# Kernel tuning notes

Measured on AMD Instinct MI355X. Metric: run time of the kernel, lower is better.

Reference implementation:

```python
import jax, jax.numpy as jnp
import numpy as np

KNN_K = 3
EPS = 1e-8


def _make_poses(key, batch):
    """Random valid SE(3) matrices [B,4,4] (rotation via QR, small translation)."""
    k1, k2 = jax.random.split(key)
    A = jax.random.normal(k1, (batch, 3, 3), dtype=jnp.float32)
    Q, _ = jnp.linalg.qr(A)
    det = jnp.linalg.det(Q)[:, None, None]
    Q = Q * jnp.where(det < 0, -1.0, 1.0)  # ensure proper rotation
    t = jax.random.normal(k2, (batch, 3), dtype=jnp.float32) * 0.5
    pose = jnp.tile(jnp.eye(4, dtype=jnp.float32), (batch, 1, 1))
    pose = pose.at[:, :3, :3].set(Q)
    pose = pose.at[:, :3, 3].set(t)
    return pose


def setup_inputs() -> dict:
    key = jax.random.key(0)
    kq, kr, kf, kp0, kp1 = jax.random.split(key, 5)
    B, N, M = 2, 8192, 8192
    pc0 = jax.random.normal(kq, (B, N, 3), dtype=jnp.float32) * 20.0
    pc1 = jax.random.normal(kr, (B, M, 3), dtype=jnp.float32) * 20.0
    flow1 = jax.random.normal(kf, (B, M, 3), dtype=jnp.float32)
    pose0 = _make_poses(kp0, B)
    pose1 = _make_poses(kp1, B)
    return {"pc0": pc0, "pc1": pc1, "flow1": flow1, "pose0": pose0, "pose1": pose1}


def reference(pc0, pc1, flow1, pose0, pose1):
    # cal_pose0to1: transform from pc0 ego frame into pc1 ego frame
    pose_0to1 = jnp.linalg.inv(pose1) @ pose0            # [B,4,4]
    R = pose_0to1[:, :3, :3]                             # [B,3,3]
    t = pose_0to1[:, :3, 3]                              # [B,3]
    # pc0_in_pc1 = pc0 @ R^T + t
    pc0_t = jnp.einsum("bij,bnj->bni", R, pc0) + t[:, None, :]  # [B,N,3]
    pose_flow = pc0_t - pc0                              # ego-motion displacement

    # pairwise squared distances (cdist^2) via GEMM form: [B,N,M]
    q2 = jnp.sum(pc0_t * pc0_t, axis=-1)                 # [B,N]
    r2 = jnp.sum(pc1 * pc1, axis=-1)                     # [B,M]
    cross = jnp.einsum("bnd,bmd->bnm", pc0_t, pc1)
    d2 = q2[:, :, None] + r2[:, None, :] - 2.0 * cross

    # KNN: k smallest distances
    neg_d2, idx = jax.lax.top_k(-d2, KNN_K)              # [B,N,k]
    d = jnp.sqrt(jnp.maximum(-neg_d2, 0.0))

    # inverse-distance weights over the k neighbors
    w = 1.0 / (d + EPS)
    w = w / jnp.sum(w, axis=-1, keepdims=True)           # [B,N,k]

    # gather neighbor flows: flow1 [B,M,3] -> [B,N,k,3]
    gathered = jnp.take_along_axis(flow1[:, None, :, :], idx[..., None], axis=2)
    flow_interp = jnp.sum(w[..., None] * gathered, axis=2)  # [B,N,3]
    return flow_interp, pose_flow
```

## Files before the change

### kernel.cpp

```cpp
#include <hip/hip_runtime.h>
#include <math.h>
#include <float.h>
#include <limits.h>

#define CS   64
#define CT   32
#define TILE_PTS (CT * CS)
#define CSP  65
#define QB1  64
#define QT   16
#define MARGIN 0.05f
typedef unsigned long long ull;
#define KMAX 0xFFFFFFFFFFFFFFFFull

__device__ __forceinline__ unsigned int ford(float f) {
    unsigned int b = __float_as_uint(f);
    return b ^ (((unsigned int)((int)b >> 31)) | 0x80000000u);
}
__device__ __forceinline__ float funord(unsigned int u) {
    unsigned int m = ((u >> 31) - 1u) | 0x80000000u;
    return __uint_as_float(u ^ m);
}

__device__ __forceinline__ ull umin64(ull a, ull b) { return a < b ? a : b; }
__device__ __forceinline__ ull umax64(ull a, ull b) { return a > b ? a : b; }

__device__ __forceinline__ void ins3k(ull k, ull& k0, ull& k1, ull& k2) {
    ull n2 = umax64(k1, umin64(k2, k));
    ull n1 = umax64(k0, umin64(k1, k));
    k0 = umin64(k0, k);
    k1 = n1;
    k2 = n2;
}

__device__ __forceinline__ void sins(float d, float& a0, float& a1, float& a2)
{
    float n1 = __builtin_amdgcn_fmed3f(a0, a1, d);
    float n2 = __builtin_amdgcn_fmed3f(a1, a2, d);
    a0 = fminf(a0, d);
    a1 = n1;
    a2 = n2;
}

__device__ __forceinline__ void pose_rel(const float* __restrict__ P0,
                                         const float* __restrict__ P1,
                                         float R[3][3], float tv[3])
{
    float dt0 = P0[3]  - P1[3];
    float dt1 = P0[7]  - P1[7];
    float dt2 = P0[11] - P1[11];
    #pragma unroll
    for (int i = 0; i < 3; ++i) {
        float a0 = P1[i], a1 = P1[4 + i], a2 = P1[8 + i];
        #pragma unroll
        for (int j = 0; j < 3; ++j)
            R[i][j] = fmaf(a2, P0[8 + j], fmaf(a1, P0[4 + j], a0 * P0[j]));
        tv[i] = fmaf(a2, dt2, fmaf(a1, dt1, a0 * dt0));
    }
}

__launch_bounds__(256, 4)
__global__ void knn_phaseA(const float* __restrict__ pc0,
                           const float* __restrict__ pc1,
                           const float* __restrict__ pose0,
                           const float* __restrict__ pose1,
                           float* __restrict__ cmin,
                           int B, int N, int M, int cstride)
{
    __shared__ float4 tile[CT * CSP];
    __shared__ float4 qd[QB1];

    const int tid = threadIdx.x;
    const int b   = blockIdx.z;
    const int ctb = blockIdx.y;
    const int qb  = blockIdx.x * QB1;
    const int pbase = ctb * TILE_PTS;

    if (tid < QB1) {
        float R[3][3], tv[3];
        pose_rel(pose0 + b * 16, pose1 + b * 16, R, tv);
        int qg0 = qb + tid;
        int qg  = (qg0 < N) ? qg0 : (N - 1);
        const float px = pc0[(size_t)(b * N + qg) * 3 + 0];
        const float py = pc0[(size_t)(b * N + qg) * 3 + 1];
        const float pz = pc0[(size_t)(b * N + qg) * 3 + 2];
        float qx = fmaf(R[0][2], pz, fmaf(R[0][1], py, R[0][0] * px)) + tv[0];
        float qy = fmaf(R[1][2], pz, fmaf(R[1][1], py, R[1][0] * px)) + tv[1];
        float qz = fmaf(R[2][2], pz, fmaf(R[2][1], py, R[2][0] * px)) + tv[2];
        qd[tid] = make_float4(qx, qy, qz,
                              (qx * qx + qy * qy) + qz * qz);
    }

    #pragma unroll
    for (int k = 0; k < TILE_PTS / (256 * 4); ++k) {
        const int pl = (tid + k * 256) * 4;
        const int p  = pbase + pl;
        float4* dst = &tile[(pl >> 6) * CSP + (pl & (CS - 1))];
        if (p + 3 < M) {
            const float4* pf = (const float4*)(pc1 + (size_t)(b * M + p) * 3);
            float4 A = pf[0], Bv = pf[1], C = pf[2];
            dst[0] = make_float4(-2.f * A.x, -2.f * A.y, -2.f * A.z,
                                 (A.x * A.x + A.y * A.y) + A.z * A.z);
            dst[1] = make_float4(-2.f * A.w, -2.f * Bv.x, -2.f * Bv.y,
                                 (A.w * A.w + Bv.x * Bv.x) + Bv.y * Bv.y);
            dst[2] = make_float4(-2.f * Bv.z, -2.f * Bv.w, -2.f * C.x,
                                 (Bv.z * Bv.z + Bv.w * Bv.w) + C.x * C.x);
            dst[3] = make_float4(-2.f * C.y, -2.f * C.z, -2.f * C.w,
                                 (C.y * C.y + C.z * C.z) + C.w * C.w);
        } else {
            #pragma unroll
            for (int u = 0; u < 4; ++u) {
                int pp = p + u;
                float4 v;
                if (pp < M) {
                    const float* s = pc1 + (size_t)(b * M + pp) * 3;
                    float x = s[0], y = s[1], z = s[2];
                    v = make_float4(-2.f * x, -2.f * y, -2.f * z,
                                    (x * x + y * y) + z * z);
                } else {
                    v = make_float4(0.f, 0.f, 0.f, FLT_MAX);
                }
                dst[u] = v;
            }
        }
    }
    __syncthreads();

    const int w    = tid >> 6;
    const int lane = tid & 63;
    const int cl   = lane & 31;
    const int part = lane >> 5;

    float4 qv[QT];
    #pragma unroll
    for (int t = 0; t < QT; ++t) qv[t] = qd[w * QT + t];

    float mm[QT];
    #pragma unroll
    for (int t = 0; t < QT; ++t) mm[t] = FLT_MAX;

    const float4* tp = &tile[cl * CSP + part * 32];
    #pragma unroll 4
    for (int i = 0; i < 32; ++i) {
        const float4 v = tp[i];
        #pragma unroll
        for (int t = 0; t < QT; ++t)
            mm[t] = fminf(mm[t],
                fmaf(qv[t].x, v.x, fmaf(qv[t].y, v.y, fmaf(qv[t].z, v.z, v.w))));
    }

    #pragma unroll
    for (int t = 0; t < QT; ++t)
        mm[t] = fminf(mm[t], __shfl_xor(mm[t], 32));

    if (part == 0) {
        const int cg = ctb * CT + cl;
        #pragma unroll
        for (int t = 0; t < QT; ++t) {
            int qg0 = qb + w * QT + t;
            int qg  = (qg0 < N) ? qg0 : (N - 1);
            cmin[((size_t)b * N + qg) * cstride + cg] = mm[t];
        }
    }
}

__launch_bounds__(256, 8)
__global__ void knn_select(const float* __restrict__ pc0,
                           const float* __restrict__ pc1,
                           const float* __restrict__ flow1,
                           const float* __restrict__ pose0,
                           const float* __restrict__ pose1,
                           const float* __restrict__ cmin,
                           float* __restrict__ out,
                           int B, int N, int M, int cstride)
{
    const int tid  = threadIdx.x;
    const int w    = tid >> 6;
    const int lane = tid & 63;
    const int g    = lane >> 4;
    const int l    = lane & 15;
    const int b    = blockIdx.y;
    const int q0   = blockIdx.x * 16 + w * 4 + g;
    const bool qvalid = (q0 < N);
    const int q    = qvalid ? q0 : (N - 1);

    const size_t row = (size_t)(b * N + q) * cstride;
    const float4 sA = *(const float4*)&cmin[row + l * 8];
    const float4 sB = *(const float4*)&cmin[row + l * 8 + 4];

    float R[3][3], tv[3];
    pose_rel(pose0 + b * 16, pose1 + b * 16, R, tv);
    const float px = pc0[(size_t)(b * N + q) * 3 + 0];
    const float py = pc0[(size_t)(b * N + q) * 3 + 1];
    const float pz = pc0[(size_t)(b * N + q) * 3 + 2];
    const float qx = fmaf(R[0][2], pz, fmaf(R[0][1], py, R[0][0] * px)) + tv[0];
    const float qy = fmaf(R[1][2], pz, fmaf(R[1][1], py, R[1][0] * px)) + tv[1];
    const float qz = fmaf(R[2][2], pz, fmaf(R[2][1], py, R[2][0] * px)) + tv[2];
    const float q2 = (qx * qx + qy * qy) + qz * qz;

    float a0 = FLT_MAX, a1 = FLT_MAX, a2 = FLT_MAX;
    sins(sA.x, a0, a1, a2); sins(sA.y, a0, a1, a2);
    sins(sA.z, a0, a1, a2); sins(sA.w, a0, a1, a2);
    sins(sB.x, a0, a1, a2); sins(sB.y, a0, a1, a2);
    sins(sB.z, a0, a1, a2); sins(sB.w, a0, a1, a2);
    #pragma unroll
    for (int msk = 1; msk <= 8; msk <<= 1) {
        float o0 = __shfl_xor(a0, msk);
        float o1 = __shfl_xor(a1, msk);
        float o2 = __shfl_xor(a2, msk);
        sins(o0, a0, a1, a2);
        sins(o1, a0, a1, a2);
        sins(o2, a0, a1, a2);
    }
    const float thr = a2 + MARGIN;

    unsigned int mbits =
          ((unsigned int)(sA.x <= thr) << 0) | ((unsigned int)(sA.y <= thr) << 1)
        | ((unsigned int)(sA.z <= thr) << 2) | ((unsigned int)(sA.w <= thr) << 3)
        | ((unsigned int)(sB.x <= thr) << 4) | ((unsigned int)(sB.y <= thr) << 5)
        | ((unsigned int)(sB.z <= thr) << 6) | ((unsigned int)(sB.w <= thr) << 7);
    ull m0 = (l < 8) ? ((ull)mbits << (8 * l)) : 0ull;
    ull m1 = (l >= 8) ? ((ull)mbits << (8 * (l - 8))) : 0ull;
    #pragma unroll
    for (int msk = 1; msk <= 8; msk <<= 1) {
        m0 |= __shfl_xor(m0, msk);
        m1 |= __shfl_xor(m1, msk);
    }

    ull kA0 = KMAX, kA1 = KMAX, kA2 = KMAX;
    ull kB0 = KMAX, kB1 = KMAX, kB2 = KMAX;
    #pragma unroll
    for (int half = 0; half < 2; ++half) {
        ull mask = half ? m1 : m0;
        const int cbase = half * 64;
        while (mask) {
            const int ck = (int)__builtin_ctzll(mask);
            mask &= mask - 1;
            const int mb = (cbase + ck) * CS;
            #pragma unroll
            for (int r = 0; r < CS / 16; ++r) {
                const int m = mb + r * 16 + l;
                if (m < M) {
                    const float* pp = pc1 + (size_t)(b * M + m) * 3;
                    float x = pp[0], y = pp[1], z = pp[2];
                    float r2 = (x * x + y * y) + z * z;
                    float cr = fmaf(qz, z, fmaf(qy, y, qx * x));
                    float dd = fmaf(-2.0f, cr, q2 + r2);
                    ull kk = ((ull)ford(dd) << 32) | (unsigned int)m;
                    if (r & 1) ins3k(kk, kB0, kB1, kB2);
                    else       ins3k(kk, kA0, kA1, kA2);
                }
            }
        }
    }
    ins3k(kB0, kA0, kA1, kA2);
    ins3k(kB1, kA0, kA1, kA2);
    ins3k(kB2, kA0, kA1, kA2);

    #pragma unroll
    for (int msk = 1; msk <= 8; msk <<= 1) {
        ull o0 = __shfl_xor(kA0, msk);
        ull o1 = __shfl_xor(kA1, msk);
        ull o2 = __shfl_xor(kA2, msk);
        ins3k(o0, kA0, kA1, kA2);
        ins3k(o1, kA0, kA1, kA2);
        ins3k(o2, kA0, kA1, kA2);
    }

    if (l == 0 && qvalid) {
        size_t pf = (size_t)B * N * 3 + (size_t)(b * N + q) * 3;
        out[pf + 0] = qx - px;
        out[pf + 1] = qy - py;
        out[pf + 2] = qz - pz;

        float D0 = funord((unsigned int)(kA0 >> 32));
        float D1 = funord((unsigned int)(kA1 >> 32));
        float D2 = funord((unsigned int)(kA2 >> 32));
        int   i0 = (int)(unsigned int)kA0;
        int   i1 = (int)(unsigned int)kA1;
        int   i2 = (int)(unsigned int)kA2;

        float dd0 = sqrtf(fmaxf(D0, 0.f));
        float dd1 = sqrtf(fmaxf(D1, 0.f));
        float dd2 = sqrtf(fmaxf(D2, 0.f));
        float w0 = 1.0f / (dd0 + 1e-8f);
        float w1 = 1.0f / (dd1 + 1e-8f);
        float w2 = 1.0f / (dd2 + 1e-8f);
        float wsum = (w0 + w1) + w2;
        w0 /= wsum; w1 /= wsum; w2 /= wsum;

        const float* f0 = flow1 + (size_t)(b * M + i0) * 3;
        const float* f1 = flow1 + (size_t)(b * M + i1) * 3;
        const float* f2 = flow1 + (size_t)(b * M + i2) * 3;

        const size_t ob = (size_t)(b * N + q) * 3;
        #pragma unroll
        for (int c = 0; c < 3; ++c) {
            float p0 = w0 * f0[c];
            float p1 = w1 * f1[c];
            float p2 = w2 * f2[c];
            out[ob + c] = (p0 + p1) + p2;
        }
    }
}

extern "C" void kernel_launch(void* const* d_in, const int* in_sizes, int n_in,
                              void* d_out, int out_size, void* d_ws, size_t ws_size,
                              hipStream_t stream) {
    const float* pc0   = (const float*)d_in[0];
    const float* pc1   = (const float*)d_in[1];
    const float* flow1 = (const float*)d_in[2];
    const float* pose0 = (const float*)d_in[3];
    const float* pose1 = (const float*)d_in[4];
    float* out = (float*)d_out;

    const int B = in_sizes[3] / 16;
    const int N = in_sizes[0] / (3 * B);
    const int M = in_sizes[1] / (3 * B);

    const int nct     = (M + TILE_PTS - 1) / TILE_PTS;
    const int cstride = nct * CT;

    float* cmin = (float*)d_ws;

    dim3 g1((N + QB1 - 1) / QB1, nct, B);
    knn_phaseA<<<g1, dim3(256), 0, stream>>>(pc0, pc1, pose0, pose1,
                                             cmin, B, N, M, cstride);

    dim3 g2((N + 15) / 16, B);
    knn_select<<<g2, dim3(256), 0, stream>>>(pc0, pc1, flow1, pose0, pose1,
                                             cmin, out, B, N, M, cstride);
}
```

Measured before the change: 34.59 us.

## Fuse KNN chunk-min and select phases into one kernel with full reference set in LDS

Replaces the two-kernel pipeline, which wrote per-chunk minima to a global workspace and then did a pruned exact search, with a single kernel. Each block loads all 8192 reference points (about 136 KB padded) into shared memory, computes chunk minima for 64 queries, picks candidate chunks, and rescans them from LDS instead of global memory. This removes the workspace round trip and the second launch. In exchange it allows only one block per CU, so grid size and occupancy drop sharply (256 blocks), and it assumes M is at most 8192.

```diff
diff --git a/kernel.cpp b/kernel.cpp
--- a/kernel.cpp
+++ b/kernel.cpp
@@ -3,15 +3,15 @@
 #include <float.h>
 #include <limits.h>
 
-#define CS   64
-#define CT   32
-#define TILE_PTS (CT * CS)
-#define CSP  65
-#define QB1  64
-#define QT   16
+#define MAXM 8192
+#define QPB  64
+#define NS   16
+#define NJ   8
+#define CLEN 64
 #define MARGIN 0.05f
 typedef unsigned long long ull;
 #define KMAX 0xFFFFFFFFFFFFFFFFull
+
 
 __device__ __forceinline__ unsigned int ford(float f) {
     unsigned int b = __float_as_uint(f);
@@ -59,45 +59,49 @@
     }
 }
 
-__launch_bounds__(256, 4)
-__global__ void knn_phaseA(const float* __restrict__ pc0,
-                           const float* __restrict__ pc1,
-                           const float* __restrict__ pose0,
-                           const float* __restrict__ pose1,
-                           float* __restrict__ cmin,
-                           int B, int N, int M, int cstride)
+__launch_bounds__(256, 1)
+__global__ void knn_fused(const float* __restrict__ pc0,
+                          const float* __restrict__ pc1,
+                          const float* __restrict__ flow1,
+                          const float* __restrict__ pose0,
+                          const float* __restrict__ pose1,
+                          float* __restrict__ out,
+                          int B, int N, int M)
 {
-    __shared__ float4 tile[CT * CSP];
-    __shared__ float4 qd[QB1];
+    __shared__ float4 tile[MAXM + (MAXM >> 4)];
+    __shared__ float4 qd[QPB];
 
     const int tid = threadIdx.x;
-    const int b   = blockIdx.z;
-    const int ctb = blockIdx.y;
-    const int qb  = blockIdx.x * QB1;
-    const int pbase = ctb * TILE_PTS;
-
-    if (tid < QB1) {
+    const int b   = blockIdx.y;
+    const int qb  = blockIdx.x * QPB;
+
+    if (tid < QPB) {
         float R[3][3], tv[3];
         pose_rel(pose0 + b * 16, pose1 + b * 16, R, tv);
         int qg0 = qb + tid;
-        int qg  = (qg0 < N) ? qg0 : (N - 1);
+        bool valid = qg0 < N;
+        int qg = valid ? qg0 : (N - 1);
         const float px = pc0[(size_t)(b * N + qg) * 3 + 0];
         const float py = pc0[(size_t)(b * N + qg) * 3 + 1];
         const float pz = pc0[(size_t)(b * N + qg) * 3 + 2];
         float qx = fmaf(R[0][2], pz, fmaf(R[0][1], py, R[0][0] * px)) + tv[0];
         float qy = fmaf(R[1][2], pz, fmaf(R[1][1], py, R[1][0] * px)) + tv[1];
         float qz = fmaf(R[2][2], pz, fmaf(R[2][1], py, R[2][0] * px)) + tv[2];
-        qd[tid] = make_float4(qx, qy, qz,
-                              (qx * qx + qy * qy) + qz * qz);
-    }
-
-    #pragma unroll
-    for (int k = 0; k < TILE_PTS / (256 * 4); ++k) {
-        const int pl = (tid + k * 256) * 4;
-        const int p  = pbase + pl;
-        float4* dst = &tile[(pl >> 6) * CSP + (pl & (CS - 1))];
-        if (p + 3 < M) {
-            const float4* pf = (const float4*)(pc1 + (size_t)(b * M + p) * 3);
+        qd[tid] = make_float4(qx, qy, qz, (qx * qx + qy * qy) + qz * qz);
+        if (valid) {
+            size_t pf = (size_t)B * N * 3 + (size_t)(b * N + qg) * 3;
+            out[pf + 0] = qx - px;
+            out[pf + 1] = qy - py;
+            out[pf + 2] = qz - pz;
+        }
+    }
+
+    #pragma unroll
+    for (int k = 0; k < MAXM / (256 * 4); ++k) {
+        const int p0 = (tid + k * 256) * 4;
+        float4* dst = &tile[p0 + (p0 >> 4)];
+        if (p0 + 3 < M) {
+            const float4* pf = (const float4*)(pc1 + (size_t)(b * M + p0) * 3);
             float4 A = pf[0], Bv = pf[1], C = pf[2];
             dst[0] = make_float4(-2.f * A.x, -2.f * A.y, -2.f * A.z,
                                  (A.x * A.x + A.y * A.y) + A.z * A.z);
@@ -110,7 +114,7 @@
         } else {
             #pragma unroll
             for (int u = 0; u < 4; ++u) {
-                int pp = p + u;
+                int pp = p0 + u;
                 float4 v;
                 if (pp < M) {
                     const float* s = pc1 + (size_t)(b * M + pp) * 3;
@@ -126,180 +130,135 @@
     }
     __syncthreads();
 
+    const int lane = tid & 63;
     const int w    = tid >> 6;
-    const int lane = tid & 63;
-    const int cl   = lane & 31;
-    const int part = lane >> 5;
-
-    float4 qv[QT];
-    #pragma unroll
-    for (int t = 0; t < QT; ++t) qv[t] = qd[w * QT + t];
-
-    float mm[QT];
-    #pragma unroll
-    for (int t = 0; t < QT; ++t) mm[t] = FLT_MAX;
-
-    const float4* tp = &tile[cl * CSP + part * 32];
-    #pragma unroll 4
-    for (int i = 0; i < 32; ++i) {
-        const float4 v = tp[i];
-        #pragma unroll
-        for (int t = 0; t < QT; ++t)
-            mm[t] = fminf(mm[t],
-                fmaf(qv[t].x, v.x, fmaf(qv[t].y, v.y, fmaf(qv[t].z, v.z, v.w))));
-    }
-
-    #pragma unroll
-    for (int t = 0; t < QT; ++t)
-        mm[t] = fminf(mm[t], __shfl_xor(mm[t], 32));
-
-    if (part == 0) {
-        const int cg = ctb * CT + cl;
-        #pragma unroll
-        for (int t = 0; t < QT; ++t) {
-            int qg0 = qb + w * QT + t;
-            int qg  = (qg0 < N) ? qg0 : (N - 1);
-            cmin[((size_t)b * N + qg) * cstride + cg] = mm[t];
-        }
-    }
-}
-
-__launch_bounds__(256, 8)
-__global__ void knn_select(const float* __restrict__ pc0,
-                           const float* __restrict__ pc1,
-                           const float* __restrict__ flow1,
-                           const float* __restrict__ pose0,
-                           const float* __restrict__ pose1,
-                           const float* __restrict__ cmin,
-                           float* __restrict__ out,
-                           int B, int N, int M, int cstride)
-{
-    const int tid  = threadIdx.x;
-    const int w    = tid >> 6;
-    const int lane = tid & 63;
+    const int s    = lane & 15;
     const int g    = lane >> 4;
-    const int l    = lane & 15;
-    const int b    = blockIdx.y;
-    const int q0   = blockIdx.x * 16 + w * 4 + g;
-    const bool qvalid = (q0 < N);
-    const int q    = qvalid ? q0 : (N - 1);
-
-    const size_t row = (size_t)(b * N + q) * cstride;
-    const float4 sA = *(const float4*)&cmin[row + l * 8];
-    const float4 sB = *(const float4*)&cmin[row + l * 8 + 4];
-
-    float R[3][3], tv[3];
-    pose_rel(pose0 + b * 16, pose1 + b * 16, R, tv);
-    const float px = pc0[(size_t)(b * N + q) * 3 + 0];
-    const float py = pc0[(size_t)(b * N + q) * 3 + 1];
-    const float pz = pc0[(size_t)(b * N + q) * 3 + 2];
-    const float qx = fmaf(R[0][2], pz, fmaf(R[0][1], py, R[0][0] * px)) + tv[0];
-    const float qy = fmaf(R[1][2], pz, fmaf(R[1][1], py, R[1][0] * px)) + tv[1];
-    const float qz = fmaf(R[2][2], pz, fmaf(R[2][1], py, R[2][0] * px)) + tv[2];
-    const float q2 = (qx * qx + qy * qy) + qz * qz;
-
-    float a0 = FLT_MAX, a1 = FLT_MAX, a2 = FLT_MAX;
-    sins(sA.x, a0, a1, a2); sins(sA.y, a0, a1, a2);
-    sins(sA.z, a0, a1, a2); sins(sA.w, a0, a1, a2);
-    sins(sB.x, a0, a1, a2); sins(sB.y, a0, a1, a2);
-    sins(sB.z, a0, a1, a2); sins(sB.w, a0, a1, a2);
-    #pragma unroll
-    for (int msk = 1; msk <= 8; msk <<= 1) {
-        float o0 = __shfl_xor(a0, msk);
-        float o1 = __shfl_xor(a1, msk);
-        float o2 = __shfl_xor(a2, msk);
-        sins(o0, a0, a1, a2);
-        sins(o1, a0, a1, a2);
-        sins(o2, a0, a1, a2);
-    }
-    const float thr = a2 + MARGIN;
-
-    unsigned int mbits =
-          ((unsigned int)(sA.x <= thr) << 0) | ((unsigned int)(sA.y <= thr) << 1)
-        | ((unsigned int)(sA.z <= thr) << 2) | ((unsigned int)(sA.w <= thr) << 3)
-        | ((unsigned int)(sB.x <= thr) << 4) | ((unsigned int)(sB.y <= thr) << 5)
-        | ((unsigned int)(sB.z <= thr) << 6) | ((unsigned int)(sB.w <= thr) << 7);
-    ull m0 = (l < 8) ? ((ull)mbits << (8 * l)) : 0ull;
-    ull m1 = (l >= 8) ? ((ull)mbits << (8 * (l - 8))) : 0ull;
-    #pragma unroll
-    for (int msk = 1; msk <= 8; msk <<= 1) {
-        m0 |= __shfl_xor(m0, msk);
-        m1 |= __shfl_xor(m1, msk);
-    }
-
-    ull kA0 = KMAX, kA1 = KMAX, kA2 = KMAX;
-    ull kB0 = KMAX, kB1 = KMAX, kB2 = KMAX;
-    #pragma unroll
-    for (int half = 0; half < 2; ++half) {
-        ull mask = half ? m1 : m0;
-        const int cbase = half * 64;
-        while (mask) {
-            const int ck = (int)__builtin_ctzll(mask);
-            mask &= mask - 1;
-            const int mb = (cbase + ck) * CS;
+    const int l    = s;
+
+    float4 qv[4];
+    #pragma unroll
+    for (int t = 0; t < 4; ++t) qv[t] = qd[w * 16 + g * 4 + t];
+
+    float mm[4][NJ];
+    #pragma unroll
+    for (int t = 0; t < 4; ++t)
+        #pragma unroll
+        for (int j = 0; j < NJ; ++j) mm[t][j] = FLT_MAX;
+
+    const float4* tp = &tile[s];
+    #pragma unroll
+    for (int j = 0; j < NJ; ++j) {
+        const float4* tpj = tp + j * (CLEN * 17);
+        #pragma unroll 4
+        for (int i = 0; i < CLEN; ++i) {
+            const float4 v = tpj[i * 17];
             #pragma unroll
-            for (int r = 0; r < CS / 16; ++r) {
-                const int m = mb + r * 16 + l;
-                if (m < M) {
-                    const float* pp = pc1 + (size_t)(b * M + m) * 3;
-                    float x = pp[0], y = pp[1], z = pp[2];
-                    float r2 = (x * x + y * y) + z * z;
-                    float cr = fmaf(qz, z, fmaf(qy, y, qx * x));
-                    float dd = fmaf(-2.0f, cr, q2 + r2);
-                    ull kk = ((ull)ford(dd) << 32) | (unsigned int)m;
+            for (int t = 0; t < 4; ++t)
+                mm[t][j] = fminf(mm[t][j],
+                    fmaf(qv[t].x, v.x, fmaf(qv[t].y, v.y, fmaf(qv[t].z, v.z, v.w))));
+        }
+    }
+
+    #pragma unroll
+    for (int t = 0; t < 4; ++t) {
+        float a0 = FLT_MAX, a1 = FLT_MAX, a2 = FLT_MAX;
+        #pragma unroll
+        for (int j = 0; j < NJ; ++j) sins(mm[t][j], a0, a1, a2);
+        #pragma unroll
+        for (int msk = 1; msk <= 8; msk <<= 1) {
+            float o0 = __shfl_xor(a0, msk);
+            float o1 = __shfl_xor(a1, msk);
+            float o2 = __shfl_xor(a2, msk);
+            sins(o0, a0, a1, a2);
+            sins(o1, a0, a1, a2);
+            sins(o2, a0, a1, a2);
+        }
+        const float thr = a2 + MARGIN;
+
+        unsigned int bits = 0;
+        #pragma unroll
+        for (int j = 0; j < NJ; ++j)
+            bits |= (unsigned int)(mm[t][j] <= thr) << j;
+        ull m0 = (s < 8) ? ((ull)bits << (8 * s)) : 0ull;
+        ull m1 = (s >= 8) ? ((ull)bits << (8 * (s - 8))) : 0ull;
+        #pragma unroll
+        for (int msk = 1; msk <= 8; msk <<= 1) {
+            m0 |= __shfl_xor(m0, msk);
+            m1 |= __shfl_xor(m1, msk);
+        }
+
+        const float4 qq = qv[t];
+        ull kA0 = KMAX, kA1 = KMAX, kA2 = KMAX;
+        ull kB0 = KMAX, kB1 = KMAX, kB2 = KMAX;
+        #pragma unroll
+        for (int half = 0; half < 2; ++half) {
+            ull mask = half ? m1 : m0;
+            const int cb = half * 64;
+            while (mask) {
+                const int c  = cb + (int)__builtin_ctzll(mask);
+                mask &= mask - 1;
+                const int sc = c >> 3;
+                const int jc = c & 7;
+                #pragma unroll
+                for (int r = 0; r < 4; ++r) {
+                    const int kk_i = jc * CLEN + r * 16 + l;
+                    const int p    = sc + 16 * kk_i;
+                    const float4 v = tile[sc + 17 * kk_i];
+                    float t2 = fmaf(qq.z, v.z, fmaf(qq.y, v.y, qq.x * v.x));
+                    float dd = (qq.w + v.w) + t2;
+                    ull kk = ((ull)ford(dd) << 32) | (unsigned int)p;
                     if (r & 1) ins3k(kk, kB0, kB1, kB2);
                     else       ins3k(kk, kA0, kA1, kA2);
                 }
             }
         }
-    }
-    ins3k(kB0, kA0, kA1, kA2);
-    ins3k(kB1, kA0, kA1, kA2);
-    ins3k(kB2, kA0, kA1, kA2);
-
-    #pragma unroll
-    for (int msk = 1; msk <= 8; msk <<= 1) {
-        ull o0 = __shfl_xor(kA0, msk);
-        ull o1 = __shfl_xor(kA1, msk);
-        ull o2 = __shfl_xor(kA2, msk);
-        ins3k(o0, kA0, kA1, kA2);
-        ins3k(o1, kA0, kA1, kA2);
-        ins3k(o2, kA0, kA1, kA2);
-    }
-
-    if (l == 0 && qvalid) {
-        size_t pf = (size_t)B * N * 3 + (size_t)(b * N + q) * 3;
-        out[pf + 0] = qx - px;
-        out[pf + 1] = qy - py;
-        out[pf + 2] = qz - pz;
-
-        float D0 = funord((unsigned int)(kA0 >> 32));
-        float D1 = funord((unsigned int)(kA1 >> 32));
-        float D2 = funord((unsigned int)(kA2 >> 32));
-        int   i0 = (int)(unsigned int)kA0;
-        int   i1 = (int)(unsigned int)kA1;
-        int   i2 = (int)(unsigned int)kA2;
-
-        float dd0 = sqrtf(fmaxf(D0, 0.f));
-        float dd1 = sqrtf(fmaxf(D1, 0.f));
-        float dd2 = sqrtf(fmaxf(D2, 0.f));
-        float w0 = 1.0f / (dd0 + 1e-8f);
-        float w1 = 1.0f / (dd1 + 1e-8f);
-        float w2 = 1.0f / (dd2 + 1e-8f);
-        float wsum = (w0 + w1) + w2;
-        w0 /= wsum; w1 /= wsum; w2 /= wsum;
-
-        const float* f0 = flow1 + (size_t)(b * M + i0) * 3;
-        const float* f1 = flow1 + (size_t)(b * M + i1) * 3;
-        const float* f2 = flow1 + (size_t)(b * M + i2) * 3;
-
-        const size_t ob = (size_t)(b * N + q) * 3;
-        #pragma unroll
-        for (int c = 0; c < 3; ++c) {
-            float p0 = w0 * f0[c];
-            float p1 = w1 * f1[c];
-            float p2 = w2 * f2[c];
-            out[ob + c] = (p0 + p1) + p2;
+        ins3k(kB0, kA0, kA1, kA2);
+        ins3k(kB1, kA0, kA1, kA2);
+        ins3k(kB2, kA0, kA1, kA2);
+
+        #pragma unroll
+        for (int msk = 1; msk <= 8; msk <<= 1) {
+            ull o0 = __shfl_xor(kA0, msk);
+            ull o1 = __shfl_xor(kA1, msk);
+            ull o2 = __shfl_xor(kA2, msk);
+            ins3k(o0, kA0, kA1, kA2);
+            ins3k(o1, kA0, kA1, kA2);
+            ins3k(o2, kA0, kA1, kA2);
+        }
+
+        if (l == 0) {
+            const int q0 = qb + w * 16 + g * 4 + t;
+            if (q0 < N) {
+                float D0 = funord((unsigned int)(kA0 >> 32));
+                float D1 = funord((unsigned int)(kA1 >> 32));
+                float D2 = funord((unsigned int)(kA2 >> 32));
+                int   i0 = (int)(unsigned int)kA0;
+                int   i1 = (int)(unsigned int)kA1;
+                int   i2 = (int)(unsigned int)kA2;
+
+                float dd0 = sqrtf(fmaxf(D0, 0.f));
+                float dd1 = sqrtf(fmaxf(D1, 0.f));
+                float dd2 = sqrtf(fmaxf(D2, 0.f));
+                float w0 = 1.0f / (dd0 + 1e-8f);
+                float w1 = 1.0f / (dd1 + 1e-8f);
+                float w2 = 1.0f / (dd2 + 1e-8f);
+                float wsum = (w0 + w1) + w2;
+                w0 /= wsum; w1 /= wsum; w2 /= wsum;
+
+                const float* f0 = flow1 + (size_t)(b * M + i0) * 3;
+                const float* f1 = flow1 + (size_t)(b * M + i1) * 3;
+                const float* f2 = flow1 + (size_t)(b * M + i2) * 3;
+
+                const size_t ob = (size_t)(b * N + q0) * 3;
+                #pragma unroll
+                for (int ch = 0; ch < 3; ++ch) {
+                    float p0 = w0 * f0[ch];
+                    float p1 = w1 * f1[ch];
+                    float p2 = w2 * f2[ch];
+                    out[ob + ch] = (p0 + p1) + p2;
+                }
+            }
         }
     }
 }
@@ -318,16 +277,7 @@
     const int N = in_sizes[0] / (3 * B);
     const int M = in_sizes[1] / (3 * B);
 
-    const int nct     = (M + TILE_PTS - 1) / TILE_PTS;
-    const int cstride = nct * CT;
-
-    float* cmin = (float*)d_ws;
-
-    dim3 g1((N + QB1 - 1) / QB1, nct, B);
-    knn_phaseA<<<g1, dim3(256), 0, stream>>>(pc0, pc1, pose0, pose1,
-                                             cmin, B, N, M, cstride);
-
-    dim3 g2((N + 15) / 16, B);
-    knn_select<<<g2, dim3(256), 0, stream>>>(pc0, pc1, flow1, pose0, pose1,
-                                             cmin, out, B, N, M, cstride);
-}
+    dim3 grid((N + QPB - 1) / QPB, B);
+    knn_fused<<<grid, dim3(256), 0, stream>>>(pc0, pc1, flow1, pose0, pose1,
+                                              out, B, N, M);
+}
```

New measurement: 40.38 us. 1.17x slower.
